# Kernel tuning notes

Hardware: AMD Instinct MI355X
Metric: run time of the kernel (lower is better)

The kernel has to match this reference:

```python
import jax, jax.numpy as jnp
import numpy as np

B = 16384      # batch
H = 1024       # latent_dim
C = 2          # output_dim (classes)
PPC = 24       # prototypes per class
P = C * PPC    # 48 total prototypes
EPS = 1e-4


def setup_inputs() -> dict:
    key = jax.random.key(0)
    k1, k2, k3, k4, k5 = jax.random.split(key, 5)
    specific_user = jax.random.normal(k1, (B, H), jnp.float32)
    shared_user = jax.random.normal(k2, (B, H), jnp.float32)
    prototype_vectors = jax.random.normal(k3, (P, H), jnp.float32)
    # last_layer weight set by set_last_layer_incorrect_connection(-0.5):
    # +1 for the prototype's own class, -0.5 elsewhere; shape [C, P]
    cls = np.arange(P) // PPC
    ident = (cls[None, :] == np.arange(C)[:, None]).astype(np.float32)
    last_layer_w = jnp.asarray(ident * 1.0 + (1.0 - ident) * (-0.5))
    # nn.Bilinear(H, H, 1): weight [1, H, H], bias [1]
    bilinear_w = jax.random.normal(k4, (1, H, H), jnp.float32) / np.sqrt(H)
    bilinear_b = jax.random.normal(k5, (1,), jnp.float32) * 0.01
    return {
        "specific_user": specific_user,
        "shared_user": shared_user,
        "prototype_vectors": prototype_vectors,
        "last_layer_w": last_layer_w,
        "bilinear_w": bilinear_w,
        "bilinear_b": bilinear_b,
        "flag": 1,
    }


def reference(specific_user, shared_user, prototype_vectors, last_layer_w,
              bilinear_w, bilinear_b, flag):
    # prototype_distances: squared euclid via mm + norms, then log-similarity
    x2 = jnp.sum(specific_user ** 2, axis=1, keepdims=True)          # [B,1]
    p2 = jnp.sum(prototype_vectors ** 2, axis=1)                     # [P]
    distance = -2.0 * (specific_user @ prototype_vectors.T) + x2 + p2[None, :]  # [B,P]
    similarity = jnp.log((distance + 1.0) / (distance + EPS))        # [B,P]
    logits = similarity @ last_layer_w.T                             # [B,C]

    # select the class's 24 prototypes (flag picks class 1 or 0; static int)
    idx = 1 if flag else 0
    sub = prototype_vectors.reshape(C, PPC, H)[idx]                  # [PPC,H]

    # prototype_subgraph_distances: per original broadcast, each row of
    # all_sim is the batch-mean of the log-similarity -> constant over batch.
    s2 = jnp.sum(sub ** 2, axis=1)                                   # [PPC]
    d = -2.0 * (specific_user @ sub.T) + x2 + s2[None, :]            # [B,PPC]
    sim = jnp.mean(jnp.log((d + 1.0) / (d + EPS)), axis=0)           # [PPC]
    jstar = jnp.argmax(sim)                                          # scalar
    chosen_proto = jnp.broadcast_to(sub[jstar], specific_user.shape) # [B,H]

    # nn.Bilinear(chosen_proto, shared_user) -> [B,1]
    pos = jnp.einsum('bi,ij,bj->b', chosen_proto, bilinear_w[0], shared_user)[:, None] + bilinear_b
    return (pos, shared_user, logits, distance)
```

## Files before the change

kernel.cpp:

```cpp
#include <hip/hip_runtime.h>
#include <hip/hip_bf16.h>

#define BATCH 16384
#define HD    1024
#define NP    48
#define PPC   24
#define EPSV  1e-4f

typedef __attribute__((ext_vector_type(8))) short  short8;
typedef __attribute__((ext_vector_type(4))) float  floatx4;

__device__ __forceinline__ float b2f(unsigned short s) {
    union { unsigned u; float f; } c; c.u = ((unsigned)s) << 16; return c.f;
}
__device__ __forceinline__ unsigned short f2bu(float f) {
    __hip_bfloat16 h = __float2bfloat16(f);
    union { __hip_bfloat16 h; unsigned short u; } c; c.h = h; return c.u;
}

__global__ __launch_bounds__(64) void k_prep(const float* __restrict__ proto,
                                             unsigned short* __restrict__ phi,
                                             unsigned short* __restrict__ plo,
                                             float* __restrict__ p2) {
    const int p = blockIdx.x;
    const int lane = threadIdx.x;
    const float* row = proto + (size_t)p * HD;
    float acc = 0.f;
    for (int k = lane; k < HD; k += 64) {
        const float f = row[k];
        acc += f * f;
        const unsigned short h = f2bu(f);
        phi[(size_t)p * HD + k] = h;
        plo[(size_t)p * HD + k] = f2bu(f - b2f(h));
    }
#pragma unroll
    for (int m = 32; m >= 1; m >>= 1) acc += __shfl_xor(acc, m, 64);
    if (lane == 0) p2[p] = acc;
}

__global__ __launch_bounds__(256, 4) void k_main(
    const float* __restrict__ x,
    const unsigned short* __restrict__ phi,
    const unsigned short* __restrict__ plo,
    const float* __restrict__ llw,
    const float* __restrict__ p2,
    float* __restrict__ gcol,
    float* __restrict__ out_logits,
    float* __restrict__ out_dist)
{
    __shared__ float lacc[4][64][13];
    __shared__ float lx2[4][16];
    const int wave = threadIdx.x >> 6;
    const int lane = threadIdx.x & 63;
    const int quad = lane >> 4;
    const int lr   = lane & 15;
    const int rb   = blockIdx.x * 16;
    const int ko   = wave * 256;

    const float* xr = x + (size_t)(rb + lr) * HD + ko + quad * 8;
    const unsigned short* ph0 = phi + (size_t)lr * HD + ko + quad * 8;
    const unsigned short* ph1 = ph0 + 16 * HD;
    const unsigned short* ph2 = ph0 + 32 * HD;
    const unsigned short* pl0 = plo + (size_t)lr * HD + ko + quad * 8;
    const unsigned short* pl1 = pl0 + 16 * HD;
    const unsigned short* pl2 = pl0 + 32 * HD;

    floatx4 acc0 = {0.f, 0.f, 0.f, 0.f};
    floatx4 acc1 = {0.f, 0.f, 0.f, 0.f};
    floatx4 acc2 = {0.f, 0.f, 0.f, 0.f};
    float x2p = 0.f;

#pragma unroll 2
    for (int kk = 0; kk < 8; ++kk) {
        const floatx4 xa = *(const floatx4*)(xr + kk * 32);
        const floatx4 xb = *(const floatx4*)(xr + kk * 32 + 4);
        short8 ah, al;
#pragma unroll
        for (int j = 0; j < 4; ++j) {
            const float f = xa[j];
            x2p += f * f;
            const unsigned short h = f2bu(f);
            ah[j] = (short)h;
            al[j] = (short)f2bu(f - b2f(h));
        }
#pragma unroll
        for (int j = 0; j < 4; ++j) {
            const float f = xb[j];
            x2p += f * f;
            const unsigned short h = f2bu(f);
            ah[4 + j] = (short)h;
            al[4 + j] = (short)f2bu(f - b2f(h));
        }
        const short8 bh0 = *(const short8*)(ph0 + kk * 32);
        const short8 bh1 = *(const short8*)(ph1 + kk * 32);
        const short8 bh2 = *(const short8*)(ph2 + kk * 32);
        const short8 bl0 = *(const short8*)(pl0 + kk * 32);
        const short8 bl1 = *(const short8*)(pl1 + kk * 32);
        const short8 bl2 = *(const short8*)(pl2 + kk * 32);
        acc0 = __builtin_amdgcn_mfma_f32_16x16x32_bf16(ah, bh0, acc0, 0, 0, 0);
        acc0 = __builtin_amdgcn_mfma_f32_16x16x32_bf16(ah, bl0, acc0, 0, 0, 0);
        acc0 = __builtin_amdgcn_mfma_f32_16x16x32_bf16(al, bh0, acc0, 0, 0, 0);
        acc1 = __builtin_amdgcn_mfma_f32_16x16x32_bf16(ah, bh1, acc1, 0, 0, 0);
        acc1 = __builtin_amdgcn_mfma_f32_16x16x32_bf16(ah, bl1, acc1, 0, 0, 0);
        acc1 = __builtin_amdgcn_mfma_f32_16x16x32_bf16(al, bh1, acc1, 0, 0, 0);
        acc2 = __builtin_amdgcn_mfma_f32_16x16x32_bf16(ah, bh2, acc2, 0, 0, 0);
        acc2 = __builtin_amdgcn_mfma_f32_16x16x32_bf16(ah, bl2, acc2, 0, 0, 0);
        acc2 = __builtin_amdgcn_mfma_f32_16x16x32_bf16(al, bh2, acc2, 0, 0, 0);
    }
    x2p += __shfl_xor(x2p, 16, 64);
    x2p += __shfl_xor(x2p, 32, 64);

#pragma unroll
    for (int r = 0; r < 4; ++r) {
        lacc[wave][lane][r]     = acc0[r];
        lacc[wave][lane][4 + r] = acc1[r];
        lacc[wave][lane][8 + r] = acc2[r];
    }
    if (quad == 0) lx2[wave][lr] = x2p;
    __syncthreads();
    if (wave != 0) return;

    float facc[12];
#pragma unroll
    for (int i = 0; i < 12; ++i)
        facc[i] = lacc[0][lane][i] + lacc[1][lane][i] + lacc[2][lane][i] + lacc[3][lane][i];
    const float x2full = lx2[0][lr] + lx2[1][lr] + lx2[2][lr] + lx2[3][lr];

    float s0[4] = {0.f, 0.f, 0.f, 0.f};
    float s1[4] = {0.f, 0.f, 0.f, 0.f};

#pragma unroll
    for (int t = 0; t < 3; ++t) {
        const int p = t * 16 + lr;
        const float p2p = p2[p];
        const float w0 = llw[p];
        const float w1 = llw[NP + p];
        float cst = 0.f;
#pragma unroll
        for (int r = 0; r < 4; ++r) {
            const int row = quad * 4 + r;
            const float x2r = __shfl(x2full, row, 64);
            const float d = -2.f * facc[t * 4 + r] + x2r + p2p;
            out_dist[(size_t)(rb + row) * NP + p] = d;
            const float sim = log1pf((1.f - EPSV) / (d + EPSV));
            s0[r] += sim * w0;
            s1[r] += sim * w1;
            cst += sim;
        }
        cst += __shfl_xor(cst, 16, 64);
        cst += __shfl_xor(cst, 32, 64);
        if (quad == 0) atomicAdd(&gcol[p], cst);
    }

#pragma unroll
    for (int r = 0; r < 4; ++r) {
        float r0 = s0[r], r1 = s1[r];
#pragma unroll
        for (int m = 1; m <= 8; m <<= 1) {
            r0 += __shfl_xor(r0, m, 64);
            r1 += __shfl_xor(r1, m, 64);
        }
        if (lr == 0) {
            const int brow = rb + quad * 4 + r;
            out_logits[(size_t)brow * 2 + 0] = r0;
            out_logits[(size_t)brow * 2 + 1] = r1;
        }
    }
}

__global__ __launch_bounds__(256) void k_matvec(
    const float* __restrict__ proto,
    const float* __restrict__ w2,
    const float* __restrict__ gcol,
    const int* __restrict__ flag,
    float* __restrict__ v)
{
    __shared__ int js;
    const int tid = threadIdx.x;
    const int idx = (flag[0] != 0) ? 1 : 0;
    if (tid == 0) {
        const float* cs = gcol + idx * PPC;
        int bj = 0; float bv = cs[0];
        for (int j = 1; j < PPC; ++j)
            if (cs[j] > bv) { bv = cs[j]; bj = j; }
        js = bj;
    }
    __syncthreads();

    const float* crow = proto + (size_t)(idx * PPC + js) * HD;
    const int i0 = blockIdx.x * 16;
    const int j4 = tid * 4;
    float a0 = 0.f, a1 = 0.f, a2 = 0.f, a3 = 0.f;
#pragma unroll 4
    for (int i = i0; i < i0 + 16; ++i) {
        const float c = crow[i];
        const floatx4 wv = *(const floatx4*)(w2 + (size_t)i * HD + j4);
        a0 += c * wv[0];
        a1 += c * wv[1];
        a2 += c * wv[2];
        a3 += c * wv[3];
    }
    atomicAdd(&v[j4 + 0], a0);
    atomicAdd(&v[j4 + 1], a1);
    atomicAdd(&v[j4 + 2], a2);
    atomicAdd(&v[j4 + 3], a3);
}

__global__ __launch_bounds__(256) void k_pos(
    const float* __restrict__ sh,
    const float* __restrict__ v,
    const float* __restrict__ bias,
    float* __restrict__ out_pos,
    float* __restrict__ out_copy)
{
    const int wave = threadIdx.x >> 6;
    const int lane = threadIdx.x & 63;
    const int b = blockIdx.x * 4 + wave;

    const floatx4* src = (const floatx4*)(sh + (size_t)b * HD);
    floatx4* dst = (floatx4*)(out_copy + (size_t)b * HD);
    const floatx4* vv = (const floatx4*)v;
    float acc = 0.f;
#pragma unroll
    for (int c = 0; c < 4; ++c) {
        const int idx = c * 64 + lane;
        const floatx4 r = src[idx];
        __builtin_nontemporal_store(r, &dst[idx]);
        const floatx4 vr = vv[idx];
#pragma unroll
        for (int j = 0; j < 4; ++j) acc += r[j] * vr[j];
    }
#pragma unroll
    for (int m = 1; m <= 32; m <<= 1) acc += __shfl_xor(acc, m, 64);
    if (lane == 0) out_pos[b] = acc + bias[0];
}

extern "C" void kernel_launch(void* const* d_in, const int* in_sizes, int n_in,
                              void* d_out, int out_size, void* d_ws, size_t ws_size,
                              hipStream_t stream) {
    const float* x     = (const float*)d_in[0];
    const float* sh    = (const float*)d_in[1];
    const float* proto = (const float*)d_in[2];
    const float* llw   = (const float*)d_in[3];
    const float* w2    = (const float*)d_in[4];
    const float* bb    = (const float*)d_in[5];
    const int*   flag  = (const int*)d_in[6];

    float* out = (float*)d_out;
    float* out_pos    = out;
    float* out_copy   = out + BATCH;
    float* out_logits = out + BATCH + BATCH * HD;
    float* out_dist   = out + BATCH + BATCH * HD + BATCH * 2;

    float* ws_v    = (float*)d_ws;
    float* ws_col  = ws_v + 1024;
    float* ws_p2   = ws_v + 1088;
    unsigned short* ws_phi = (unsigned short*)(ws_v + 16384);
    unsigned short* ws_plo = ws_phi + NP * HD;

    hipMemsetAsync(d_ws, 0, 8192, stream);
    k_prep<<<48, 64, 0, stream>>>(proto, ws_phi, ws_plo, ws_p2);
    k_main<<<1024, 256, 0, stream>>>(x, ws_phi, ws_plo, llw, ws_p2, ws_col, out_logits, out_dist);
    k_matvec<<<64, 256, 0, stream>>>(proto, w2, ws_col, flag, ws_v);
    k_pos<<<4096, 256, 0, stream>>>(sh, ws_v, bb, out_pos, out_copy);
}
```

Before: 228.3 us.

## Precompute bilinear matvec for all candidate prototypes in prep kernel; drop matvec launch

The prep kernel now also computes W·p for all 24 candidate prototypes of the selected class, so the argmax-dependent matvec no longer sits between the main and pos kernels. The pos kernel does the argmax itself and indexes the precomputed row. The memset and the separate matvec launch are removed, and gcol is zeroed inside prep. This trades about 24x more matvec work, done off the critical dependency chain, for two fewer launches and serial steps.

```diff
diff --git a/kernel.cpp b/kernel.cpp
--- a/kernel.cpp
+++ b/kernel.cpp
@@ -18,24 +18,56 @@
     union { __hip_bfloat16 h; unsigned short u; } c; c.h = h; return c.u;
 }
 
-__global__ __launch_bounds__(64) void k_prep(const float* __restrict__ proto,
-                                             unsigned short* __restrict__ phi,
-                                             unsigned short* __restrict__ plo,
-                                             float* __restrict__ p2) {
-    const int p = blockIdx.x;
-    const int lane = threadIdx.x;
-    const float* row = proto + (size_t)p * HD;
-    float acc = 0.f;
-    for (int k = lane; k < HD; k += 64) {
-        const float f = row[k];
-        acc += f * f;
-        const unsigned short h = f2bu(f);
-        phi[(size_t)p * HD + k] = h;
-        plo[(size_t)p * HD + k] = f2bu(f - b2f(h));
-    }
-#pragma unroll
-    for (int m = 32; m >= 1; m >>= 1) acc += __shfl_xor(acc, m, 64);
-    if (lane == 0) p2[p] = acc;
+__global__ __launch_bounds__(256) void k_prep(const float* __restrict__ proto,
+                                              const float* __restrict__ w2,
+                                              const int*   __restrict__ flag,
+                                              unsigned short* __restrict__ phi,
+                                              unsigned short* __restrict__ plo,
+                                              float* __restrict__ p2,
+                                              float* __restrict__ gcol,
+                                              float* __restrict__ V) {
+    const int bid = blockIdx.x;
+    const int tid = threadIdx.x;
+
+    if (bid < 48) {
+        const int p = bid;
+        if (p == 4 && tid < NP) gcol[tid] = 0.f;
+        const float* row = proto + (size_t)p * HD;
+        float acc = 0.f;
+#pragma unroll
+        for (int c = 0; c < 4; ++c) {
+            const int k = c * 256 + tid;
+            const float f = row[k];
+            acc += f * f;
+            const unsigned short h = f2bu(f);
+            phi[(size_t)p * HD + k] = h;
+            plo[(size_t)p * HD + k] = f2bu(f - b2f(h));
+        }
+#pragma unroll
+        for (int m = 32; m >= 1; m >>= 1) acc += __shfl_xor(acc, m, 64);
+        __shared__ float wsum[4];
+        if ((tid & 63) == 0) wsum[tid >> 6] = acc;
+        __syncthreads();
+        if (tid == 0) p2[p] = wsum[0] + wsum[1] + wsum[2] + wsum[3];
+    } else {
+        const int q   = bid - 48;
+        const int jg  = q >> 4;
+        const int cc  = q & 15;
+        const int c   = cc * 64 + (tid & 63);
+        const int j   = jg * 4 + (tid >> 6);
+        const int idx = (flag[0] != 0) ? 1 : 0;
+        const float* prow = proto + (size_t)(idx * PPC + j) * HD;
+        float acc = 0.f;
+#pragma unroll 2
+        for (int i = 0; i < HD; i += 4) {
+            const floatx4 pv = *(const floatx4*)(prow + i);
+            acc += pv[0] * w2[(size_t)(i + 0) * HD + c];
+            acc += pv[1] * w2[(size_t)(i + 1) * HD + c];
+            acc += pv[2] * w2[(size_t)(i + 2) * HD + c];
+            acc += pv[3] * w2[(size_t)(i + 3) * HD + c];
+        }
+        V[(size_t)j * HD + c] = acc;
+    }
 }
 
 __global__ __launch_bounds__(256, 4) void k_main(
@@ -168,17 +200,19 @@
     }
 }
 
-__global__ __launch_bounds__(256) void k_matvec(
-    const float* __restrict__ proto,
-    const float* __restrict__ w2,
+__global__ __launch_bounds__(256) void k_pos(
+    const float* __restrict__ sh,
+    const float* __restrict__ V,
     const float* __restrict__ gcol,
-    const int* __restrict__ flag,
-    float* __restrict__ v)
+    const int*   __restrict__ flag,
+    const float* __restrict__ bias,
+    float* __restrict__ out_pos,
+    float* __restrict__ out_copy)
 {
     __shared__ int js;
-    const int tid = threadIdx.x;
-    const int idx = (flag[0] != 0) ? 1 : 0;
+    const int tid  = threadIdx.x;
     if (tid == 0) {
+        const int idx = (flag[0] != 0) ? 1 : 0;
         const float* cs = gcol + idx * PPC;
         int bj = 0; float bv = cs[0];
         for (int j = 1; j < PPC; ++j)
@@ -187,46 +221,20 @@
     }
     __syncthreads();
 
-    const float* crow = proto + (size_t)(idx * PPC + js) * HD;
-    const int i0 = blockIdx.x * 16;
-    const int j4 = tid * 4;
-    float a0 = 0.f, a1 = 0.f, a2 = 0.f, a3 = 0.f;
-#pragma unroll 4
-    for (int i = i0; i < i0 + 16; ++i) {
-        const float c = crow[i];
-        const floatx4 wv = *(const floatx4*)(w2 + (size_t)i * HD + j4);
-        a0 += c * wv[0];
-        a1 += c * wv[1];
-        a2 += c * wv[2];
-        a3 += c * wv[3];
-    }
-    atomicAdd(&v[j4 + 0], a0);
-    atomicAdd(&v[j4 + 1], a1);
-    atomicAdd(&v[j4 + 2], a2);
-    atomicAdd(&v[j4 + 3], a3);
-}
-
-__global__ __launch_bounds__(256) void k_pos(
-    const float* __restrict__ sh,
-    const float* __restrict__ v,
-    const float* __restrict__ bias,
-    float* __restrict__ out_pos,
-    float* __restrict__ out_copy)
-{
-    const int wave = threadIdx.x >> 6;
-    const int lane = threadIdx.x & 63;
+    const int wave = tid >> 6;
+    const int lane = tid & 63;
     const int b = blockIdx.x * 4 + wave;
 
     const floatx4* src = (const floatx4*)(sh + (size_t)b * HD);
     floatx4* dst = (floatx4*)(out_copy + (size_t)b * HD);
-    const floatx4* vv = (const floatx4*)v;
+    const floatx4* vv = (const floatx4*)(V + (size_t)js * HD);
     float acc = 0.f;
 #pragma unroll
     for (int c = 0; c < 4; ++c) {
-        const int idx = c * 64 + lane;
-        const floatx4 r = src[idx];
-        __builtin_nontemporal_store(r, &dst[idx]);
-        const floatx4 vr = vv[idx];
+        const int idx2 = c * 64 + lane;
+        const floatx4 r = src[idx2];
+        __builtin_nontemporal_store(r, &dst[idx2]);
+        const floatx4 vr = vv[idx2];
 #pragma unroll
         for (int j = 0; j < 4; ++j) acc += r[j] * vr[j];
     }
@@ -252,15 +260,13 @@
     float* out_logits = out + BATCH + BATCH * HD;
     float* out_dist   = out + BATCH + BATCH * HD + BATCH * 2;
 
-    float* ws_v    = (float*)d_ws;
-    float* ws_col  = ws_v + 1024;
-    float* ws_p2   = ws_v + 1088;
-    unsigned short* ws_phi = (unsigned short*)(ws_v + 16384);
+    float* ws_col = (float*)d_ws;
+    float* ws_p2  = ws_col + 64;
+    float* ws_V   = ws_col + 1024;
+    unsigned short* ws_phi = (unsigned short*)(ws_col + 25600);
     unsigned short* ws_plo = ws_phi + NP * HD;
 
-    hipMemsetAsync(d_ws, 0, 8192, stream);
-    k_prep<<<48, 64, 0, stream>>>(proto, ws_phi, ws_plo, ws_p2);
+    k_prep<<<144, 256, 0, stream>>>(proto, w2, flag, ws_phi, ws_plo, ws_p2, ws_col, ws_V);
     k_main<<<1024, 256, 0, stream>>>(x, ws_phi, ws_plo, llw, ws_p2, ws_col, out_logits, out_dist);
-    k_matvec<<<64, 256, 0, stream>>>(proto, w2, ws_col, flag, ws_v);
-    k_pos<<<4096, 256, 0, stream>>>(sh, ws_v, bb, out_pos, out_copy);
-}
+    k_pos<<<4096, 256, 0, stream>>>(sh, ws_V, ws_col, flag, bb, out_pos, out_copy);
+}
```

New measurement: 282.6 us. 23.8% more time.
